# Kernel optimization log

Hardware: AMD Instinct MI355X
Metric: run time of the kernel (lower is better)

The kernel has to match this reference:

```python
import jax, jax.numpy as jnp
import numpy as np

D_MODEL, D_FF, N_EXPERTS, N_TASKS, K_TOP = 512, 2048, 8, 4, 2
B, N = 8, 1024


def setup_inputs() -> dict:
    key = jax.random.key(0)
    ks = jax.random.split(key, 16)
    s = lambda *sh: 1.0 / np.sqrt(sh[-2] if len(sh) > 1 else sh[-1])
    inp = {
        "x": jax.random.normal(ks[0], (B, N, D_MODEL), jnp.float32),
        "task_ids": jax.random.randint(ks[1], (B,), 0, N_TASKS),
        "task_embed": jax.random.normal(ks[2], (N_TASKS, D_MODEL), jnp.float32),
        "gate_w": jax.random.normal(ks[3], (2 * D_MODEL, N_EXPERTS), jnp.float32) * 0.02,
        "gate_b": jnp.zeros((N_EXPERTS,), jnp.float32),
        "w1": jax.random.normal(ks[4], (N_EXPERTS, D_MODEL, D_FF), jnp.float32) * (1.0 / np.sqrt(D_MODEL)),
        "b1": jnp.zeros((N_EXPERTS, D_FF), jnp.float32),
        "w2": jax.random.normal(ks[5], (N_EXPERTS, D_FF, D_MODEL), jnp.float32) * (1.0 / np.sqrt(D_FF)),
        "b2": jnp.zeros((N_EXPERTS, D_MODEL), jnp.float32),
        "uw1": jax.random.normal(ks[6], (D_MODEL, D_FF), jnp.float32) * (1.0 / np.sqrt(D_MODEL)),
        "ub1": jnp.zeros((D_FF,), jnp.float32),
        "uw2": jax.random.normal(ks[7], (D_FF, D_MODEL), jnp.float32) * (1.0 / np.sqrt(D_FF)),
        "ub2": jnp.zeros((D_MODEL,), jnp.float32),
    }
    return inp


def _moe_forward(x, task_ids, task_embed, gate_w, gate_b, w1, b1, w2, b2, uw1, ub1, uw2, ub2):
    Bc, Nc, Dc = x.shape
    E = gate_b.shape[0]
    # task-conditioned gating
    t_vec = task_embed[task_ids]                              # [B, D]
    t_bcast = jnp.broadcast_to(t_vec[:, None, :], (Bc, Nc, Dc))
    gate_in = jnp.concatenate([x, t_bcast], axis=-1)          # [B, N, 2D]
    logits = gate_in @ gate_w + gate_b                        # [B, N, E]
    # top-k gating: softmax over top-k logits, zero elsewhere
    k = min(K_TOP, E)
    topk_vals, topk_idx = jax.lax.top_k(logits, k)            # [B, N, k]
    probs = jax.nn.softmax(topk_vals, axis=-1)                # [B, N, k]
    gates = jnp.sum(jax.nn.one_hot(topk_idx, E, dtype=x.dtype) * probs[..., None], axis=-2)  # [B, N, E]
    # dense expert compute (all experts on all tokens, as in reference)
    h = jnp.einsum("bnd,edf->benf", x, w1) + b1[None, :, None, :]     # [B, E, N, F]
    h = jax.nn.gelu(h, approximate=False)
    eo = jnp.einsum("benf,efd->bend", h, w2) + b2[None, :, None, :]    # [B, E, N, D]
    task_out = jnp.einsum("bne,bend->bnd", gates, eo)                  # [B, N, D]
    # universal expert
    uh = jax.nn.gelu(x @ uw1 + ub1, approximate=False)
    univ = uh @ uw2 + ub2                                              # [B, N, D]
    omega = 1.0 - jnp.max(gates, axis=-1, keepdims=True)               # [B, N, 1]
    out = task_out + omega * univ
    return out, logits


def reference(x, task_ids, task_embed, gate_w, gate_b, w1, b1, w2, b2, uw1, ub1, uw2, ub2):
    return _moe_forward(x, task_ids, task_embed, gate_w, gate_b, w1, b1, w2, b2, uw1, ub1, uw2, ub2)
```

## Files before the change

### kernel.cpp

```cpp
#include <hip/hip_runtime.h>

#define D_MODEL 512
#define D_FF    2048
#define NEXP    8
#define TOKENS  8192
#define TROWS   26368

typedef __bf16 bf16_t;
typedef __attribute__((ext_vector_type(8))) __bf16 bf16x8_t;
typedef __attribute__((ext_vector_type(4))) __bf16 bf16x4_t;
typedef __attribute__((ext_vector_type(4))) float  f32x4_t;

#define W1P_OFF    0u
#define UW1P_OFF   16777216u
#define W2P_OFF    18874368u
#define UW2P_OFF   35651584u
#define CNT_OFF    37748736u
#define TOKL_OFF   37748800u
#define GATEL_OFF  38010944u
#define OMEGA_OFF  38273088u
#define TLOG_OFF   38305856u
#define SOFF_OFF   38306368u
#define SPC_OFF    38306432u
#define RMETA_OFF  38306496u
#define RGATE_OFF  38411968u
#define XGP_OFF    38517440u
#define S0_OFF     38517440u
#define S1_OFF     46906048u
#define HP_OFF     65517248u
#define TOKE_OFF   173516480u
#define TG_OFF     173549248u
#define TMAP_OFF   173614784u

__device__ inline f32x4_t mfma_bf16(bf16x8_t a, bf16x8_t b, f32x4_t c) {
  return __builtin_amdgcn_mfma_f32_16x16x32_bf16(a, b, c, 0, 0, 0);
}

__device__ __forceinline__ void load_lds16(const void* g, void* l) {
  __builtin_amdgcn_global_load_lds(
      (const __attribute__((address_space(1))) unsigned int*)g,
      (__attribute__((address_space(3))) unsigned int*)l, 16, 0, 0);
}

__device__ __forceinline__ float fast_gelu(float x) {
  float z = 0.7978845608f * (x + 0.044715f * x * x * x);
  float u = __expf(2.0f * z);
  float th = (u - 1.0f) * __builtin_amdgcn_rcpf(u + 1.0f);
  return 0.5f * x * (1.0f + th);
}

__global__ void k_pack(const float* __restrict__ in, bf16_t* __restrict__ out, int R, int C) {
  const size_t mat = (size_t)blockIdx.z * R * C;
  in  += mat;
  out += mat;
  int r0 = blockIdx.y * 64, c0 = blockIdx.x * 64;
  int item = threadIdx.x >> 1, jh = threadIdx.x & 1;
  int c = item & 63, s = item >> 6;
  const float* src = in + (size_t)(r0 + s * 32 + jh * 16) * C + (c0 + c);
  union { bf16_t h[16]; uint4 u[2]; } t;
#pragma unroll
  for (int k = 0; k < 16; k++) t.h[k] = (bf16_t)src[(size_t)k * C];
  char* dst = (char*)out + ((size_t)((r0 >> 5) + s) * C + (c0 + c)) * 64 + jh * 32;
  ((uint4*)dst)[0] = t.u[0];
  ((uint4*)dst)[1] = t.u[1];
}

__global__ void k_tlog(const int* __restrict__ task_ids, const float* __restrict__ task_emb,
                       const float* __restrict__ gate_w, const float* __restrict__ gate_b,
                       double* __restrict__ tlog) {
  int i = threadIdx.x;
  if (i >= 64) return;
  int b = i >> 3, e = i & 7;
  const float* te = task_emb + (size_t)task_ids[b] * D_MODEL;
  double acc = (double)gate_b[e];
  for (int d = 0; d < D_MODEL; d++)
    acc += (double)te[d] * (double)gate_w[(size_t)(D_MODEL + d) * NEXP + e];
  tlog[i] = acc;
}

__global__ void k_gate(const float* __restrict__ x, const float* __restrict__ gate_w,
                       const double* __restrict__ tlog,
                       float* __restrict__ logits_out,
                       int* __restrict__ toke, float2* __restrict__ tg,
                       float* __restrict__ omega) {
  int gtid = blockIdx.x * blockDim.x + threadIdx.x;
  int t = gtid >> 6;
  int lane = gtid & 63;
  if (t >= TOKENS) return;
  const float* xr = x + (size_t)t * D_MODEL;
  int d0 = lane * 8;
  float4 xa = *(const float4*)(xr + d0);
  float4 xc = *(const float4*)(xr + d0 + 4);
  float xv[8] = {xa.x, xa.y, xa.z, xa.w, xc.x, xc.y, xc.z, xc.w};
  double acc[NEXP];
#pragma unroll
  for (int e = 0; e < NEXP; e++) acc[e] = 0.0;
#pragma unroll
  for (int j = 0; j < 8; j++) {
    const float* gwr = gate_w + (size_t)(d0 + j) * NEXP;
    float4 g0 = *(const float4*)gwr;
    float4 g1 = *(const float4*)(gwr + 4);
    double xd = (double)xv[j];
    acc[0] += xd * (double)g0.x; acc[1] += xd * (double)g0.y;
    acc[2] += xd * (double)g0.z; acc[3] += xd * (double)g0.w;
    acc[4] += xd * (double)g1.x; acc[5] += xd * (double)g1.y;
    acc[6] += xd * (double)g1.z; acc[7] += xd * (double)g1.w;
  }
#pragma unroll
  for (int off = 32; off > 0; off >>= 1) {
#pragma unroll
    for (int e = 0; e < NEXP; e++) acc[e] += __shfl_xor(acc[e], off);
  }
  if (lane == 0) {
    int b = t >> 10;
    double lg[NEXP];
#pragma unroll
    for (int e = 0; e < NEXP; e++) {
      lg[e] = acc[e] + tlog[b * NEXP + e];
      logits_out[(size_t)t * NEXP + e] = (float)lg[e];
    }
    int e0 = 0;
    for (int e = 1; e < NEXP; e++) if (lg[e] > lg[e0]) e0 = e;
    int e1 = (e0 == 0) ? 1 : 0;
    for (int e = 0; e < NEXP; e++) if (e != e0 && lg[e] > lg[e1]) e1 = e;
    double p0 = 1.0 / (1.0 + exp(lg[e1] - lg[e0]));
    float g0f = (float)p0;
    float g1f = (float)(1.0 - p0);
    omega[t] = 1.0f - g0f;
    toke[t] = e0 | (e1 << 8);
    tg[t] = float2{g0f, g1f};
  }
}

__global__ void k_route(const int* __restrict__ toke, const float2* __restrict__ tg,
                        int* __restrict__ counts, int* __restrict__ tokl,
                        float* __restrict__ gatel) {
  __shared__ int lcnt[NEXP];
  __shared__ int lbase[NEXP];
  const int tid = threadIdx.x;
  if (tid < NEXP) lcnt[tid] = 0;
  __syncthreads();
  const int t = blockIdx.x * 256 + tid;
  const int pe = toke[t];
  const int e0 = pe & 0xff, e1 = pe >> 8;
  const float2 g = tg[t];
  const int r0 = atomicAdd(&lcnt[e0], 1);
  const int r1 = atomicAdd(&lcnt[e1], 1);
  __syncthreads();
  if (tid < NEXP) lbase[tid] = atomicAdd(counts + tid, lcnt[tid]);
  __syncthreads();
  int i0 = lbase[e0] + r0;
  tokl[e0 * TOKENS + i0]  = (t << 1);
  gatel[e0 * TOKENS + i0] = g.x;
  int i1 = lbase[e1] + r1;
  tokl[e1 * TOKENS + i1]  = (t << 1) | 1;
  gatel[e1 * TOKENS + i1] = g.y;
}

__global__ void k_soff(const int* __restrict__ cnts, int* __restrict__ soff,
                       int* __restrict__ spc, int* __restrict__ tmap) {
  if (threadIdx.x == 0) {
    soff[8] = 0; spc[8] = TOKENS;
    int n = 0;
    for (int mt = 0; mt < 32; mt++) tmap[n++] = (8 << 8) | mt;
    int off = TOKENS;
    for (int e = 0; e < 8; e++) {
      int c = cnts[e];
      int p = (c + 255) & ~255;
      soff[e] = off; spc[e] = p;
      off += p;
      for (int mt = 0; mt < (p >> 8); mt++) tmap[n++] = (e << 8) | mt;
    }
    tmap[128] = n;
  }
}

__global__ void k_fill(const int* __restrict__ cnts, const int* __restrict__ soff,
                       const int* __restrict__ spc,
                       const int* __restrict__ tokl, const float* __restrict__ gatel,
                       const float* __restrict__ omega,
                       int* __restrict__ rmeta, float* __restrict__ rgate) {
  int r = blockIdx.x * 256 + threadIdx.x;
  if (r >= TROWS) return;
  if (r < TOKENS) { rmeta[r] = (r << 2) | 2; rgate[r] = omega[r]; return; }
  int meta = 3; float g = 0.f;
#pragma unroll
  for (int e = 0; e < 8; e++) {
    int off = soff[e];
    if (r >= off && r < off + spc[e]) {
      int i = r - off;
      if (i < cnts[e]) {
        int en = tokl[e * TOKENS + i];
        meta = ((en >> 1) << 2) | (en & 1);
        g = gatel[e * TOKENS + i];
      }
      break;
    }
  }
  rmeta[r] = meta; rgate[r] = g;
}

__global__ void k_gather(const float* __restrict__ x, const int* __restrict__ rmeta,
                         bf16_t* __restrict__ xgp) {
  int rbase = blockIdx.x * 128;
  for (int it = 0; it < 8; it++) {
    int id = it * 256 + threadIdx.x;
    int row = rbase + (id >> 4), s = id & 15;
    int meta = rmeta[row];
    union { bf16_t h[32]; uint4 u[4]; } t;
    if ((meta & 3) == 3) {
#pragma unroll
      for (int j = 0; j < 4; j++) t.u[j] = uint4{0, 0, 0, 0};
    } else {
      const float* src = x + (size_t)(meta >> 2) * D_MODEL + s * 32;
#pragma unroll
      for (int j = 0; j < 32; j += 4) {
        float4 v = *(const float4*)(src + j);
        t.h[j] = (bf16_t)v.x; t.h[j + 1] = (bf16_t)v.y;
        t.h[j + 2] = (bf16_t)v.z; t.h[j + 3] = (bf16_t)v.w;
      }
    }
    char* dst = (char*)xgp + ((size_t)s * TROWS + row) * 64;
#pragma unroll
    for (int j = 0; j < 4; j++) ((uint4*)dst)[j] = t.u[j];
  }
}

template <int KT, int NB, int EPI, int NT, int LOG2NT>
__global__ __launch_bounds__(512, 4) void k_gemm(
    const bf16_t* __restrict__ Ab, const bf16_t* __restrict__ wEx,
    const bf16_t* __restrict__ wUn, const float* __restrict__ bEx,
    const float* __restrict__ bUn,
    const int* __restrict__ soff, const int* __restrict__ tmap,
    bf16_t* __restrict__ hpOut,
    const int* __restrict__ rmeta, const float* __restrict__ rgate,
    bf16_t* __restrict__ s0, bf16_t* __restrict__ s1, float* __restrict__ outF) {
  const int wg = blockIdx.x;
  const int xcd = wg & 7, j = wg >> 3;
  const int t = xcd + ((j >> LOG2NT) << 3);
  const int nt = j & (NT - 1);
  if (t >= tmap[128]) return;
  const int tm = tmap[t];
  const int sec = tm >> 8, mt = tm & 255;

  const int groff = soff[sec];
  const char* Bsec = (const char*)((sec == 8) ? wUn : (wEx + (size_t)sec * KT * NB * 32));
  const float* bias = (sec == 8) ? bUn : (bEx + sec * NB);

  __shared__ char smem[73728];
  const int tid = threadIdx.x;
  const int wave = tid >> 6, lane = tid & 63;
  const int l16 = lane & 15, quad = lane >> 4;
  const int wm = wave >> 1, wn = wave & 1;

  const int r0 = tid >> 2;
  const int ss = (tid & 3) ^ ((tid >> 3) & 3);
  const int grow0 = groff + mt * 256;
  const char* aSrc = (const char*)Ab + (size_t)(grow0 + r0) * 64 + ss * 16;
  const char* bSrc = Bsec + (size_t)(nt * 128 + r0) * 64 + ss * 16;
  char* ldsWA = smem + wave * 1024;
  char* ldsWB = smem + 49152 + wave * 1024;

  const int swz = ((quad ^ ((l16 >> 1) & 3)) << 4);
  const int aRd = (wm * 64 + l16) * 64 + swz;
  const int bRd = (wn * 64 + l16) * 64 + swz;

  f32x4_t acc[4][4];
#pragma unroll
  for (int i = 0; i < 4; i++)
#pragma unroll
    for (int n = 0; n < 4; n++) acc[i][n] = f32x4_t{0.f, 0.f, 0.f, 0.f};

  auto stage = [&](int kt, int set) {
    const char* ga = aSrc + (size_t)kt * ((size_t)TROWS * 64);
    char* la = ldsWA + set * 16384;
    load_lds16(ga, la);
    load_lds16(ga + 8192, la + 8192);
    load_lds16(bSrc + (size_t)kt * ((size_t)NB * 64), ldsWB + set * 8192);
  };

  stage(0, 0); stage(1, 1);
  asm volatile("s_waitcnt vmcnt(3)" ::: "memory");
  __builtin_amdgcn_s_barrier();

  int rs = 0, ws = 2;
  for (int kt = 0; kt < KT; ++kt) {
    const char* abase = smem + rs * 16384;
    const char* bbase = smem + 49152 + rs * 8192;
    bf16x8_t Ar[4], Br[4];
#pragma unroll
    for (int f = 0; f < 4; f++) Ar[f] = *(const bf16x8_t*)(abase + aRd + f * 1024);
#pragma unroll
    for (int f = 0; f < 4; f++) Br[f] = *(const bf16x8_t*)(bbase + bRd + f * 1024);
    if (kt < KT - 2) stage(kt + 2, ws);
    asm volatile("s_waitcnt lgkmcnt(0)" ::: "memory");
    __builtin_amdgcn_sched_barrier(0);
    __builtin_amdgcn_s_setprio(1);
#pragma unroll
    for (int mm = 0; mm < 4; mm++)
#pragma unroll
      for (int n = 0; n < 4; n++)
        acc[mm][n] = mfma_bf16(Br[n], Ar[mm], acc[mm][n]);
    __builtin_amdgcn_s_setprio(0);
    if (kt < KT - 2)       asm volatile("s_waitcnt vmcnt(3)" ::: "memory");
    else if (kt == KT - 2) asm volatile("s_waitcnt vmcnt(0)" ::: "memory");
    if (kt < KT - 1) __builtin_amdgcn_s_barrier();
    if (++rs == 3) rs = 0;
    if (++ws == 3) ws = 0;
  }

  const int colq = wn * 64 + quad * 4;
  float4 bv[4];
#pragma unroll
  for (int n = 0; n < 4; n++)
    bv[n] = *(const float4*)(bias + nt * 128 + colq + n * 16);

  if constexpr (EPI == 0) {
#pragma unroll
    for (int mm = 0; mm < 4; mm++) {
      const int row = grow0 + wm * 64 + mm * 16 + l16;
#pragma unroll
      for (int n = 0; n < 4; n++) {
        float b4[4] = {bv[n].x, bv[n].y, bv[n].z, bv[n].w};
        union { bf16_t h[4]; uint2 u; } t2;
#pragma unroll
        for (int i = 0; i < 4; i++)
          t2.h[i] = (bf16_t)fast_gelu(acc[mm][n][i] + b4[i]);
        char* dst = (char*)hpOut +
            ((size_t)(nt * 4 + wn * 2 + (n >> 1)) * TROWS + row) * 64 +
            (n & 1) * 32 + quad * 8;
        *(uint2*)dst = t2.u;
      }
    }
  } else {
#pragma unroll
    for (int mm = 0; mm < 4; mm++) {
      const int grow = grow0 + wm * 64 + mm * 16 + l16;
      const int dbase = nt * 128 + colq;
      if (sec == 8) {
        const float g = rgate[grow];
        float* dst = outF + (size_t)grow * D_MODEL + dbase;
#pragma unroll
        for (int n = 0; n < 4; n++) {
          float b4[4] = {bv[n].x, bv[n].y, bv[n].z, bv[n].w};
          float4 o;
          o.x = (acc[mm][n][0] + b4[0]) * g;
          o.y = (acc[mm][n][1] + b4[1]) * g;
          o.z = (acc[mm][n][2] + b4[2]) * g;
          o.w = (acc[mm][n][3] + b4[3]) * g;
          *(float4*)(dst + n * 16) = o;
        }
      } else {
        const int meta = rmeta[grow];
        const int slot = meta & 3;
        if (slot == 3) continue;
        const float g = rgate[grow];
        bf16_t* dst = (slot ? s1 : s0) + (size_t)(meta >> 2) * D_MODEL + dbase;
#pragma unroll
        for (int n = 0; n < 4; n++) {
          float b4[4] = {bv[n].x, bv[n].y, bv[n].z, bv[n].w};
          union { bf16_t h[4]; uint2 u; } t2;
#pragma unroll
          for (int i = 0; i < 4; i++)
            t2.h[i] = (bf16_t)((acc[mm][n][i] + b4[i]) * g);
          *(uint2*)(dst + n * 16) = t2.u;
        }
      }
    }
  }
}

__global__ void k_combine(const bf16x4_t* __restrict__ s0, const bf16x4_t* __restrict__ s1,
                          float4* __restrict__ out, int n4) {
  int i = blockIdx.x * blockDim.x + threadIdx.x;
  if (i >= n4) return;
  bf16x4_t a = s0[i], b = s1[i];
  float4 o = out[i];
  o.x += (float)a[0] + (float)b[0];
  o.y += (float)a[1] + (float)b[1];
  o.z += (float)a[2] + (float)b[2];
  o.w += (float)a[3] + (float)b[3];
  out[i] = o;
}

extern "C" void kernel_launch(void* const* d_in, const int* in_sizes, int n_in,
                              void* d_out, int out_size, void* d_ws, size_t ws_size,
                              hipStream_t stream) {
  (void)in_sizes; (void)n_in; (void)out_size; (void)ws_size;
  const float* x        = (const float*)d_in[0];
  const int*   task_ids = (const int*)  d_in[1];
  const float* task_emb = (const float*)d_in[2];
  const float* gate_w   = (const float*)d_in[3];
  const float* gate_b   = (const float*)d_in[4];
  const float* w1       = (const float*)d_in[5];
  const float* b1       = (const float*)d_in[6];
  const float* w2       = (const float*)d_in[7];
  const float* b2       = (const float*)d_in[8];
  const float* uw1      = (const float*)d_in[9];
  const float* ub1      = (const float*)d_in[10];
  const float* uw2      = (const float*)d_in[11];
  const float* ub2      = (const float*)d_in[12];

  char* ws = (char*)d_ws;
  bf16_t* w1p   = (bf16_t*)(ws + W1P_OFF);
  bf16_t* uw1p  = (bf16_t*)(ws + UW1P_OFF);
  bf16_t* w2p   = (bf16_t*)(ws + W2P_OFF);
  bf16_t* uw2p  = (bf16_t*)(ws + UW2P_OFF);
  bf16_t* s0    = (bf16_t*)(ws + S0_OFF);
  bf16_t* s1    = (bf16_t*)(ws + S1_OFF);
  int*    cnts  = (int*)   (ws + CNT_OFF);
  int*    tokl  = (int*)   (ws + TOKL_OFF);
  float*  gatel = (float*) (ws + GATEL_OFF);
  float*  omg   = (float*) (ws + OMEGA_OFF);
  double* tlog  = (double*)(ws + TLOG_OFF);
  int*    soff  = (int*)   (ws + SOFF_OFF);
  int*    spc   = (int*)   (ws + SPC_OFF);
  int*    rmeta = (int*)   (ws + RMETA_OFF);
  float*  rgate = (float*) (ws + RGATE_OFF);
  bf16_t* xgp   = (bf16_t*)(ws + XGP_OFF);
  bf16_t* hp    = (bf16_t*)(ws + HP_OFF);
  int*    toke  = (int*)   (ws + TOKE_OFF);
  float2* tg    = (float2*)(ws + TG_OFF);
  int*    tmap  = (int*)   (ws + TMAP_OFF);

  float* out    = (float*)d_out;
  float* logits = out + (size_t)TOKENS * D_MODEL;

  hipMemsetAsync(cnts, 0, 64, stream);

  k_pack<<<dim3(32, 8, NEXP), 256, 0, stream>>>(w1, w1p, D_MODEL, D_FF);
  k_pack<<<dim3(8, 32, NEXP), 256, 0, stream>>>(w2, w2p, D_FF, D_MODEL);
  k_pack<<<dim3(32, 8, 1),    256, 0, stream>>>(uw1, uw1p, D_MODEL, D_FF);
  k_pack<<<dim3(8, 32, 1),    256, 0, stream>>>(uw2, uw2p, D_FF, D_MODEL);
  k_tlog<<<1, 64, 0, stream>>>(task_ids, task_emb, gate_w, gate_b, tlog);
  k_gate<<<dim3(TOKENS / 4), 256, 0, stream>>>(x, gate_w, tlog, logits, toke, tg, omg);
  k_route<<<dim3(TOKENS / 256), 256, 0, stream>>>(toke, tg, cnts, tokl, gatel);
  k_soff<<<1, 64, 0, stream>>>(cnts, soff, spc, tmap);
  k_fill<<<dim3((TROWS + 255) / 256), 256, 0, stream>>>(cnts, soff, spc, tokl, gatel, omg,
                                                        rmeta, rgate);
  k_gather<<<dim3(TROWS / 128), 256, 0, stream>>>(x, rmeta, xgp);
  k_gemm<16, D_FF, 0, 16, 4><<<dim3(104 * 16), 512, 0, stream>>>(
      xgp, w1p, uw1p, b1, ub1, soff, tmap, hp,
      nullptr, nullptr, nullptr, nullptr, nullptr);
  k_gemm<64, D_MODEL, 1, 4, 2><<<dim3(104 * 4), 512, 0, stream>>>(
      hp, w2p, uw2p, b2, ub2, soff, tmap, nullptr,
      rmeta, rgate, s0, s1, out);
  const int n4 = TOKENS * D_MODEL / 4;
  k_combine<<<dim3(n4 / 256), 256, 0, stream>>>((const bf16x4_t*)s0, (const bf16x4_t*)s1,
                                                (float4*)out, n4);
}
```

Before: 375.7 us.

## Split-K second GEMM with atomic float accumulation, drop combine, merge pack launches

The second expert GEMM is split along K into two halves so twice as many workgroups run. Each writes its gated partial result straight into the zero-initialised output with float atomicAdd, which removes the bf16 staging buffers and the combine kernel. The GEMM pipeline shrinks from triple to double buffering with less LDS, the four weight-pack launches become two, and the task-logit kernel gets a parallel reduction. The cost is many scalar atomics, an extra memset of the output, a full vmcnt(0) wait on every k-step, and a summation order that is no longer deterministic.

```diff
diff --git a/kernel.cpp b/kernel.cpp
--- a/kernel.cpp
+++ b/kernel.cpp
@@ -8,7 +8,6 @@
 
 typedef __bf16 bf16_t;
 typedef __attribute__((ext_vector_type(8))) __bf16 bf16x8_t;
-typedef __attribute__((ext_vector_type(4))) __bf16 bf16x4_t;
 typedef __attribute__((ext_vector_type(4))) float  f32x4_t;
 
 #define W1P_OFF    0u
@@ -25,8 +24,6 @@
 #define RMETA_OFF  38306496u
 #define RGATE_OFF  38411968u
 #define XGP_OFF    38517440u
-#define S0_OFF     38517440u
-#define S1_OFF     46906048u
 #define HP_OFF     65517248u
 #define TOKE_OFF   173516480u
 #define TG_OFF     173549248u
@@ -49,10 +46,11 @@
   return 0.5f * x * (1.0f + th);
 }
 
-__global__ void k_pack(const float* __restrict__ in, bf16_t* __restrict__ out, int R, int C) {
-  const size_t mat = (size_t)blockIdx.z * R * C;
-  in  += mat;
-  out += mat;
+__global__ void k_pack(const float* __restrict__ wE, const float* __restrict__ wU,
+                       bf16_t* __restrict__ oE, bf16_t* __restrict__ oU, int R, int C) {
+  const int z = blockIdx.z;
+  const float* in = (z < 8) ? wE + (size_t)z * R * C : wU;
+  bf16_t* out     = (z < 8) ? oE + (size_t)z * R * C : oU;
   int r0 = blockIdx.y * 64, c0 = blockIdx.x * 64;
   int item = threadIdx.x >> 1, jh = threadIdx.x & 1;
   int c = item & 63, s = item >> 6;
@@ -68,14 +66,21 @@
 __global__ void k_tlog(const int* __restrict__ task_ids, const float* __restrict__ task_emb,
                        const float* __restrict__ gate_w, const float* __restrict__ gate_b,
                        double* __restrict__ tlog) {
-  int i = threadIdx.x;
-  if (i >= 64) return;
+  __shared__ double red[64][8];
+  int i = threadIdx.x >> 3, ch = threadIdx.x & 7;
   int b = i >> 3, e = i & 7;
   const float* te = task_emb + (size_t)task_ids[b] * D_MODEL;
-  double acc = (double)gate_b[e];
-  for (int d = 0; d < D_MODEL; d++)
+  double acc = 0.0;
+  for (int d = ch * 64; d < ch * 64 + 64; d++)
     acc += (double)te[d] * (double)gate_w[(size_t)(D_MODEL + d) * NEXP + e];
-  tlog[i] = acc;
+  red[i][ch] = acc;
+  __syncthreads();
+  if (ch == 0) {
+    double s = (double)gate_b[e];
+#pragma unroll
+    for (int k = 0; k < 8; k++) s += red[i][k];
+    tlog[i] = s;
+  }
 }
 
 __global__ void k_gate(const float* __restrict__ x, const float* __restrict__ gate_w,
@@ -226,7 +231,7 @@
   }
 }
 
-template <int KT, int NB, int EPI, int NT, int LOG2NT>
+template <int KT, int NB, int EPI, int NT, int LOG2NT, int LOG2KS>
 __global__ __launch_bounds__(512, 4) void k_gemm(
     const bf16_t* __restrict__ Ab, const bf16_t* __restrict__ wEx,
     const bf16_t* __restrict__ wUn, const float* __restrict__ bEx,
@@ -234,20 +239,24 @@
     const int* __restrict__ soff, const int* __restrict__ tmap,
     bf16_t* __restrict__ hpOut,
     const int* __restrict__ rmeta, const float* __restrict__ rgate,
-    bf16_t* __restrict__ s0, bf16_t* __restrict__ s1, float* __restrict__ outF) {
+    float* __restrict__ outF) {
   const int wg = blockIdx.x;
   const int xcd = wg & 7, j = wg >> 3;
-  const int t = xcd + ((j >> LOG2NT) << 3);
   const int nt = j & (NT - 1);
+  const int ksp = (j >> LOG2NT) & ((1 << LOG2KS) - 1);
+  const int trow = j >> (LOG2NT + LOG2KS);
+  const int t = xcd + (trow << 3);
   if (t >= tmap[128]) return;
   const int tm = tmap[t];
   const int sec = tm >> 8, mt = tm & 255;
+  const int koff = ksp * KT;
+  constexpr int KTOT = KT << LOG2KS;
 
   const int groff = soff[sec];
-  const char* Bsec = (const char*)((sec == 8) ? wUn : (wEx + (size_t)sec * KT * NB * 32));
+  const char* Bsec = (const char*)((sec == 8) ? wUn : (wEx + (size_t)sec * KTOT * NB * 32));
   const float* bias = (sec == 8) ? bUn : (bEx + sec * NB);
 
-  __shared__ char smem[73728];
+  __shared__ char smem[49152];
   const int tid = threadIdx.x;
   const int wave = tid >> 6, lane = tid & 63;
   const int l16 = lane & 15, quad = lane >> 4;
@@ -256,10 +265,12 @@
   const int r0 = tid >> 2;
   const int ss = (tid & 3) ^ ((tid >> 3) & 3);
   const int grow0 = groff + mt * 256;
-  const char* aSrc = (const char*)Ab + (size_t)(grow0 + r0) * 64 + ss * 16;
-  const char* bSrc = Bsec + (size_t)(nt * 128 + r0) * 64 + ss * 16;
+  const char* aSrc = (const char*)Ab + (size_t)(grow0 + r0) * 64 + ss * 16 +
+                     (size_t)koff * ((size_t)TROWS * 64);
+  const char* bSrc = Bsec + (size_t)(nt * 128 + r0) * 64 + ss * 16 +
+                     (size_t)koff * ((size_t)NB * 64);
   char* ldsWA = smem + wave * 1024;
-  char* ldsWB = smem + 49152 + wave * 1024;
+  char* ldsWB = smem + 32768 + wave * 1024;
 
   const int swz = ((quad ^ ((l16 >> 1) & 3)) << 4);
   const int aRd = (wm * 64 + l16) * 64 + swz;
@@ -279,20 +290,20 @@
     load_lds16(bSrc + (size_t)kt * ((size_t)NB * 64), ldsWB + set * 8192);
   };
 
-  stage(0, 0); stage(1, 1);
-  asm volatile("s_waitcnt vmcnt(3)" ::: "memory");
+  stage(0, 0);
+  asm volatile("s_waitcnt vmcnt(0)" ::: "memory");
   __builtin_amdgcn_s_barrier();
 
-  int rs = 0, ws = 2;
   for (int kt = 0; kt < KT; ++kt) {
+    const int rs = kt & 1;
+    if (kt < KT - 1) stage(kt + 1, rs ^ 1);
     const char* abase = smem + rs * 16384;
-    const char* bbase = smem + 49152 + rs * 8192;
+    const char* bbase = smem + 32768 + rs * 8192;
     bf16x8_t Ar[4], Br[4];
 #pragma unroll
     for (int f = 0; f < 4; f++) Ar[f] = *(const bf16x8_t*)(abase + aRd + f * 1024);
 #pragma unroll
     for (int f = 0; f < 4; f++) Br[f] = *(const bf16x8_t*)(bbase + bRd + f * 1024);
-    if (kt < KT - 2) stage(kt + 2, ws);
     asm volatile("s_waitcnt lgkmcnt(0)" ::: "memory");
     __builtin_amdgcn_sched_barrier(0);
     __builtin_amdgcn_s_setprio(1);
@@ -302,11 +313,10 @@
       for (int n = 0; n < 4; n++)
         acc[mm][n] = mfma_bf16(Br[n], Ar[mm], acc[mm][n]);
     __builtin_amdgcn_s_setprio(0);
-    if (kt < KT - 2)       asm volatile("s_waitcnt vmcnt(3)" ::: "memory");
-    else if (kt == KT - 2) asm volatile("s_waitcnt vmcnt(0)" ::: "memory");
-    if (kt < KT - 1) __builtin_amdgcn_s_barrier();
-    if (++rs == 3) rs = 0;
-    if (++ws == 3) ws = 0;
+    if (kt < KT - 1) {
+      asm volatile("s_waitcnt vmcnt(0)" ::: "memory");
+      __builtin_amdgcn_s_barrier();
+    }
   }
 
   const int colq = wn * 64 + quad * 4;
@@ -314,6 +324,10 @@
 #pragma unroll
   for (int n = 0; n < 4; n++)
     bv[n] = *(const float4*)(bias + nt * 128 + colq + n * 16);
+  if (LOG2KS > 0 && ksp != 0) {
+#pragma unroll
+    for (int n = 0; n < 4; n++) bv[n] = float4{0.f, 0.f, 0.f, 0.f};
+  }
 
   if constexpr (EPI == 0) {
 #pragma unroll
@@ -336,51 +350,19 @@
 #pragma unroll
     for (int mm = 0; mm < 4; mm++) {
       const int grow = grow0 + wm * 64 + mm * 16 + l16;
-      const int dbase = nt * 128 + colq;
-      if (sec == 8) {
-        const float g = rgate[grow];
-        float* dst = outF + (size_t)grow * D_MODEL + dbase;
-#pragma unroll
-        for (int n = 0; n < 4; n++) {
-          float b4[4] = {bv[n].x, bv[n].y, bv[n].z, bv[n].w};
-          float4 o;
-          o.x = (acc[mm][n][0] + b4[0]) * g;
-          o.y = (acc[mm][n][1] + b4[1]) * g;
-          o.z = (acc[mm][n][2] + b4[2]) * g;
-          o.w = (acc[mm][n][3] + b4[3]) * g;
-          *(float4*)(dst + n * 16) = o;
-        }
-      } else {
-        const int meta = rmeta[grow];
-        const int slot = meta & 3;
-        if (slot == 3) continue;
-        const float g = rgate[grow];
-        bf16_t* dst = (slot ? s1 : s0) + (size_t)(meta >> 2) * D_MODEL + dbase;
-#pragma unroll
-        for (int n = 0; n < 4; n++) {
-          float b4[4] = {bv[n].x, bv[n].y, bv[n].z, bv[n].w};
-          union { bf16_t h[4]; uint2 u; } t2;
-#pragma unroll
-          for (int i = 0; i < 4; i++)
-            t2.h[i] = (bf16_t)((acc[mm][n][i] + b4[i]) * g);
-          *(uint2*)(dst + n * 16) = t2.u;
-        }
+      const int meta = rmeta[grow];
+      if ((meta & 3) == 3) continue;
+      const float g = rgate[grow];
+      float* dst = outF + (size_t)(meta >> 2) * D_MODEL + nt * 128 + colq;
+#pragma unroll
+      for (int n = 0; n < 4; n++) {
+        float b4[4] = {bv[n].x, bv[n].y, bv[n].z, bv[n].w};
+#pragma unroll
+        for (int i = 0; i < 4; i++)
+          atomicAdd(dst + n * 16 + i, (acc[mm][n][i] + b4[i]) * g);
       }
     }
   }
-}
-
-__global__ void k_combine(const bf16x4_t* __restrict__ s0, const bf16x4_t* __restrict__ s1,
-                          float4* __restrict__ out, int n4) {
-  int i = blockIdx.x * blockDim.x + threadIdx.x;
-  if (i >= n4) return;
-  bf16x4_t a = s0[i], b = s1[i];
-  float4 o = out[i];
-  o.x += (float)a[0] + (float)b[0];
-  o.y += (float)a[1] + (float)b[1];
-  o.z += (float)a[2] + (float)b[2];
-  o.w += (float)a[3] + (float)b[3];
-  out[i] = o;
 }
 
 extern "C" void kernel_launch(void* const* d_in, const int* in_sizes, int n_in,
@@ -406,8 +388,6 @@
   bf16_t* uw1p  = (bf16_t*)(ws + UW1P_OFF);
   bf16_t* w2p   = (bf16_t*)(ws + W2P_OFF);
   bf16_t* uw2p  = (bf16_t*)(ws + UW2P_OFF);
-  bf16_t* s0    = (bf16_t*)(ws + S0_OFF);
-  bf16_t* s1    = (bf16_t*)(ws + S1_OFF);
   int*    cnts  = (int*)   (ws + CNT_OFF);
   int*    tokl  = (int*)   (ws + TOKL_OFF);
   float*  gatel = (float*) (ws + GATEL_OFF);
@@ -427,25 +407,19 @@
   float* logits = out + (size_t)TOKENS * D_MODEL;
 
   hipMemsetAsync(cnts, 0, 64, stream);
-
-  k_pack<<<dim3(32, 8, NEXP), 256, 0, stream>>>(w1, w1p, D_MODEL, D_FF);
-  k_pack<<<dim3(8, 32, NEXP), 256, 0, stream>>>(w2, w2p, D_FF, D_MODEL);
-  k_pack<<<dim3(32, 8, 1),    256, 0, stream>>>(uw1, uw1p, D_MODEL, D_FF);
-  k_pack<<<dim3(8, 32, 1),    256, 0, stream>>>(uw2, uw2p, D_FF, D_MODEL);
-  k_tlog<<<1, 64, 0, stream>>>(task_ids, task_emb, gate_w, gate_b, tlog);
+  hipMemsetAsync(out, 0, (size_t)TOKENS * D_MODEL * 4, stream);
+
+  k_pack<<<dim3(32, 8, 9), 256, 0, stream>>>(w1, uw1, w1p, uw1p, D_MODEL, D_FF);
+  k_pack<<<dim3(8, 32, 9), 256, 0, stream>>>(w2, uw2, w2p, uw2p, D_FF, D_MODEL);
+  k_tlog<<<1, 512, 0, stream>>>(task_ids, task_emb, gate_w, gate_b, tlog);
   k_gate<<<dim3(TOKENS / 4), 256, 0, stream>>>(x, gate_w, tlog, logits, toke, tg, omg);
   k_route<<<dim3(TOKENS / 256), 256, 0, stream>>>(toke, tg, cnts, tokl, gatel);
   k_soff<<<1, 64, 0, stream>>>(cnts, soff, spc, tmap);
   k_fill<<<dim3((TROWS + 255) / 256), 256, 0, stream>>>(cnts, soff, spc, tokl, gatel, omg,
                                                         rmeta, rgate);
   k_gather<<<dim3(TROWS / 128), 256, 0, stream>>>(x, rmeta, xgp);
-  k_gemm<16, D_FF, 0, 16, 4><<<dim3(104 * 16), 512, 0, stream>>>(
-      xgp, w1p, uw1p, b1, ub1, soff, tmap, hp,
-      nullptr, nullptr, nullptr, nullptr, nullptr);
-  k_gemm<64, D_MODEL, 1, 4, 2><<<dim3(104 * 4), 512, 0, stream>>>(
-      hp, w2p, uw2p, b2, ub2, soff, tmap, nullptr,
-      rmeta, rgate, s0, s1, out);
-  const int n4 = TOKENS * D_MODEL / 4;
-  k_combine<<<dim3(n4 / 256), 256, 0, stream>>>((const bf16x4_t*)s0, (const bf16x4_t*)s1,
-                                                (float4*)out, n4);
-}
+  k_gemm<16, D_FF, 0, 16, 4, 0><<<dim3(104 * 16), 512, 0, stream>>>(
+      xgp, w1p, uw1p, b1, ub1, soff, tmap, hp, nullptr, nullptr, nullptr);
+  k_gemm<32, D_MODEL, 1, 4, 2, 1><<<dim3(104 * 4 * 2), 512, 0, stream>>>(
+      hp, w2p, uw2p, b2, ub2, soff, tmap, nullptr, rmeta, rgate, out);
+}
```

New measurement: 655.0 us. 1.74x slower.

## Merge pack/route launches, parallelize tlog, and move GEMM prefetch earlier

Applied to the files above, without the earlier changes.

Merges the expert and universal weight packing into one launch per matrix. Fuses the offset, fill and gather kernels into a single kernel that computes segment offsets per block and keeps row metadata in LDS. Splits the task-logit reduction across 512 threads. In the GEMM main loop, the next-stage global-to-LDS prefetch is issued before the LDS fragment reads, and the lgkmcnt wait moves after the MFMAs. These changes cut launch count and serial tiny-kernel latency, and aim for better load/compute overlap, at some risk of changed scheduling and LDS hazards in the GEMM.

```diff
diff --git a/kernel.cpp b/kernel.cpp
--- a/kernel.cpp
+++ b/kernel.cpp
@@ -21,7 +21,6 @@
 #define OMEGA_OFF  38273088u
 #define TLOG_OFF   38305856u
 #define SOFF_OFF   38306368u
-#define SPC_OFF    38306432u
 #define RMETA_OFF  38306496u
 #define RGATE_OFF  38411968u
 #define XGP_OFF    38517440u
@@ -49,10 +48,11 @@
   return 0.5f * x * (1.0f + th);
 }
 
-__global__ void k_pack(const float* __restrict__ in, bf16_t* __restrict__ out, int R, int C) {
-  const size_t mat = (size_t)blockIdx.z * R * C;
-  in  += mat;
-  out += mat;
+__global__ void k_pack(const float* __restrict__ wE, const float* __restrict__ wU,
+                       bf16_t* __restrict__ oE, bf16_t* __restrict__ oU, int R, int C) {
+  const int z = blockIdx.z;
+  const float* in = (z < 8) ? wE + (size_t)z * R * C : wU;
+  bf16_t* out     = (z < 8) ? oE + (size_t)z * R * C : oU;
   int r0 = blockIdx.y * 64, c0 = blockIdx.x * 64;
   int item = threadIdx.x >> 1, jh = threadIdx.x & 1;
   int c = item & 63, s = item >> 6;
@@ -68,14 +68,21 @@
 __global__ void k_tlog(const int* __restrict__ task_ids, const float* __restrict__ task_emb,
                        const float* __restrict__ gate_w, const float* __restrict__ gate_b,
                        double* __restrict__ tlog) {
-  int i = threadIdx.x;
-  if (i >= 64) return;
+  __shared__ double red[64][8];
+  int i = threadIdx.x >> 3, ch = threadIdx.x & 7;
   int b = i >> 3, e = i & 7;
   const float* te = task_emb + (size_t)task_ids[b] * D_MODEL;
-  double acc = (double)gate_b[e];
-  for (int d = 0; d < D_MODEL; d++)
+  double acc = 0.0;
+  for (int d = ch * 64; d < ch * 64 + 64; d++)
     acc += (double)te[d] * (double)gate_w[(size_t)(D_MODEL + d) * NEXP + e];
-  tlog[i] = acc;
+  red[i][ch] = acc;
+  __syncthreads();
+  if (ch == 0) {
+    double s = (double)gate_b[e];
+#pragma unroll
+    for (int k = 0; k < 8; k++) s += red[i][k];
+    tlog[i] = s;
+  }
 }
 
 __global__ void k_gate(const float* __restrict__ x, const float* __restrict__ gate_w,
@@ -157,56 +164,61 @@
   gatel[e1 * TOKENS + i1] = g.y;
 }
 
-__global__ void k_soff(const int* __restrict__ cnts, int* __restrict__ soff,
-                       int* __restrict__ spc, int* __restrict__ tmap) {
-  if (threadIdx.x == 0) {
-    soff[8] = 0; spc[8] = TOKENS;
-    int n = 0;
-    for (int mt = 0; mt < 32; mt++) tmap[n++] = (8 << 8) | mt;
+__global__ void k_fillgather(const float* __restrict__ x, const int* __restrict__ cnts,
+                             const int* __restrict__ tokl, const float* __restrict__ gatel,
+                             const float* __restrict__ omega,
+                             int* __restrict__ rmeta, float* __restrict__ rgate,
+                             int* __restrict__ soff_g, int* __restrict__ tmap,
+                             bf16_t* __restrict__ xgp) {
+  __shared__ int lmeta[128];
+  const int tid = threadIdx.x;
+  const int rbase = blockIdx.x * 128;
+  int so[8], sp[8];
+  {
     int off = TOKENS;
+#pragma unroll
     for (int e = 0; e < 8; e++) {
       int c = cnts[e];
       int p = (c + 255) & ~255;
-      soff[e] = off; spc[e] = p;
-      off += p;
-      for (int mt = 0; mt < (p >> 8); mt++) tmap[n++] = (e << 8) | mt;
-    }
+      so[e] = off; sp[e] = p; off += p;
+    }
+  }
+  if (tid < 128) {
+    int r = rbase + tid;
+    int meta = 3; float g = 0.f;
+    if (r < TOKENS) { meta = (r << 2) | 2; g = omega[r]; }
+    else {
+#pragma unroll
+      for (int e = 0; e < 8; e++) {
+        if (r >= so[e] && r < so[e] + sp[e]) {
+          int i = r - so[e];
+          if (i < cnts[e]) {
+            int en = tokl[e * TOKENS + i];
+            meta = ((en >> 1) << 2) | (en & 1);
+            g = gatel[e * TOKENS + i];
+          }
+          break;
+        }
+      }
+    }
+    rmeta[r] = meta; rgate[r] = g; lmeta[tid] = meta;
+  }
+  if (blockIdx.x == 0 && tid == 255) {
+    int n = 0;
+    for (int mt = 0; mt < 32; mt++) tmap[n++] = (8 << 8) | mt;
+    for (int e = 0; e < 8; e++) {
+      soff_g[e] = so[e];
+      for (int mt = 0; mt < (sp[e] >> 8); mt++) tmap[n++] = (e << 8) | mt;
+    }
+    soff_g[8] = 0;
     tmap[128] = n;
   }
-}
-
-__global__ void k_fill(const int* __restrict__ cnts, const int* __restrict__ soff,
-                       const int* __restrict__ spc,
-                       const int* __restrict__ tokl, const float* __restrict__ gatel,
-                       const float* __restrict__ omega,
-                       int* __restrict__ rmeta, float* __restrict__ rgate) {
-  int r = blockIdx.x * 256 + threadIdx.x;
-  if (r >= TROWS) return;
-  if (r < TOKENS) { rmeta[r] = (r << 2) | 2; rgate[r] = omega[r]; return; }
-  int meta = 3; float g = 0.f;
-#pragma unroll
-  for (int e = 0; e < 8; e++) {
-    int off = soff[e];
-    if (r >= off && r < off + spc[e]) {
-      int i = r - off;
-      if (i < cnts[e]) {
-        int en = tokl[e * TOKENS + i];
-        meta = ((en >> 1) << 2) | (en & 1);
-        g = gatel[e * TOKENS + i];
-      }
-      break;
-    }
-  }
-  rmeta[r] = meta; rgate[r] = g;
-}
-
-__global__ void k_gather(const float* __restrict__ x, const int* __restrict__ rmeta,
-                         bf16_t* __restrict__ xgp) {
-  int rbase = blockIdx.x * 128;
+  __syncthreads();
+#pragma unroll
   for (int it = 0; it < 8; it++) {
-    int id = it * 256 + threadIdx.x;
-    int row = rbase + (id >> 4), s = id & 15;
-    int meta = rmeta[row];
+    int id = it * 256 + tid;
+    int lrow = id >> 4, s = id & 15;
+    int meta = lmeta[lrow];
     union { bf16_t h[32]; uint4 u[4]; } t;
     if ((meta & 3) == 3) {
 #pragma unroll
@@ -220,7 +232,7 @@
         t.h[j + 2] = (bf16_t)v.z; t.h[j + 3] = (bf16_t)v.w;
       }
     }
-    char* dst = (char*)xgp + ((size_t)s * TROWS + row) * 64;
+    char* dst = (char*)xgp + ((size_t)s * TROWS + rbase + lrow) * 64;
 #pragma unroll
     for (int j = 0; j < 4; j++) ((uint4*)dst)[j] = t.u[j];
   }
@@ -285,6 +297,7 @@
 
   int rs = 0, ws = 2;
   for (int kt = 0; kt < KT; ++kt) {
+    if (kt < KT - 2) stage(kt + 2, ws);
     const char* abase = smem + rs * 16384;
     const char* bbase = smem + 49152 + rs * 8192;
     bf16x8_t Ar[4], Br[4];
@@ -292,9 +305,6 @@
     for (int f = 0; f < 4; f++) Ar[f] = *(const bf16x8_t*)(abase + aRd + f * 1024);
 #pragma unroll
     for (int f = 0; f < 4; f++) Br[f] = *(const bf16x8_t*)(bbase + bRd + f * 1024);
-    if (kt < KT - 2) stage(kt + 2, ws);
-    asm volatile("s_waitcnt lgkmcnt(0)" ::: "memory");
-    __builtin_amdgcn_sched_barrier(0);
     __builtin_amdgcn_s_setprio(1);
 #pragma unroll
     for (int mm = 0; mm < 4; mm++)
@@ -302,6 +312,7 @@
       for (int n = 0; n < 4; n++)
         acc[mm][n] = mfma_bf16(Br[n], Ar[mm], acc[mm][n]);
     __builtin_amdgcn_s_setprio(0);
+    asm volatile("s_waitcnt lgkmcnt(0)" ::: "memory");
     if (kt < KT - 2)       asm volatile("s_waitcnt vmcnt(3)" ::: "memory");
     else if (kt == KT - 2) asm volatile("s_waitcnt vmcnt(0)" ::: "memory");
     if (kt < KT - 1) __builtin_amdgcn_s_barrier();
@@ -414,7 +425,6 @@
   float*  omg   = (float*) (ws + OMEGA_OFF);
   double* tlog  = (double*)(ws + TLOG_OFF);
   int*    soff  = (int*)   (ws + SOFF_OFF);
-  int*    spc   = (int*)   (ws + SPC_OFF);
   int*    rmeta = (int*)   (ws + RMETA_OFF);
   float*  rgate = (float*) (ws + RGATE_OFF);
   bf16_t* xgp   = (bf16_t*)(ws + XGP_OFF);
@@ -428,17 +438,13 @@
 
   hipMemsetAsync(cnts, 0, 64, stream);
 
-  k_pack<<<dim3(32, 8, NEXP), 256, 0, stream>>>(w1, w1p, D_MODEL, D_FF);
-  k_pack<<<dim3(8, 32, NEXP), 256, 0, stream>>>(w2, w2p, D_FF, D_MODEL);
-  k_pack<<<dim3(32, 8, 1),    256, 0, stream>>>(uw1, uw1p, D_MODEL, D_FF);
-  k_pack<<<dim3(8, 32, 1),    256, 0, stream>>>(uw2, uw2p, D_FF, D_MODEL);
-  k_tlog<<<1, 64, 0, stream>>>(task_ids, task_emb, gate_w, gate_b, tlog);
+  k_pack<<<dim3(32, 8, 9), 256, 0, stream>>>(w1, uw1, w1p, uw1p, D_MODEL, D_FF);
+  k_pack<<<dim3(8, 32, 9), 256, 0, stream>>>(w2, uw2, w2p, uw2p, D_FF, D_MODEL);
+  k_tlog<<<1, 512, 0, stream>>>(task_ids, task_emb, gate_w, gate_b, tlog);
   k_gate<<<dim3(TOKENS / 4), 256, 0, stream>>>(x, gate_w, tlog, logits, toke, tg, omg);
   k_route<<<dim3(TOKENS / 256), 256, 0, stream>>>(toke, tg, cnts, tokl, gatel);
-  k_soff<<<1, 64, 0, stream>>>(cnts, soff, spc, tmap);
-  k_fill<<<dim3((TROWS + 255) / 256), 256, 0, stream>>>(cnts, soff, spc, tokl, gatel, omg,
-                                                        rmeta, rgate);
-  k_gather<<<dim3(TROWS / 128), 256, 0, stream>>>(x, rmeta, xgp);
+  k_fillgather<<<dim3(TROWS / 128), 256, 0, stream>>>(x, cnts, tokl, gatel, omg,
+                                                      rmeta, rgate, soff, tmap, xgp);
   k_gemm<16, D_FF, 0, 16, 4><<<dim3(104 * 16), 512, 0, stream>>>(
       xgp, w1p, uw1p, b1, ub1, soff, tmap, hp,
       nullptr, nullptr, nullptr, nullptr, nullptr);
```

After: 344.2 us. 1.09x faster.
